# Optimization experiments

Hardware: AMD Instinct MI355X
Metric: run time of the kernel (lower is better)

Reference implementation:

```python
import jax, jax.numpy as jnp
import numpy as np

B, C, L, K, R = 32, 64, 16384, 3, 8

def _lrelu(x):
    return jnp.where(x >= 0, x, 0.1 * x)

def setup_inputs() -> dict:
    key = jax.random.key(0)
    ks = jax.random.split(key, 8)
    s = lambda i, shape: (jax.random.normal(ks[i], shape, jnp.float32) * 0.05)
    return {
        "x0": jax.random.normal(ks[0], (B, C, L), jnp.float32),
        "x1": jax.random.normal(ks[1], (B, 64), jnp.float32),
        "W1": s(2, (64, 64)),           # Linear(64,64).weight [out,in]
        "W2": s(3, (64 * K, 64)),       # Linear(64,64*K).weight
        "conv_w": s(4, (C, C)),         # 1x1 Conv1d weight [out,in]
        "conv_b": s(5, (C,)),
        "ca_w1": s(6, (C // R, C)),     # CA conv1 weight
        "ca_w2": s(7, (C, C // R)),     # CA conv2 weight
    }

def reference(x0, x1, W1, W2, conv_w, conv_b, ca_w1, ca_w2):
    b, c, l = x0.shape
    k = W2.shape[0] // 64
    pad = (k - 1) // 2
    # dynamic per-(b,c) depthwise kernels
    h = _lrelu(x1 @ W1.T)                         # [b,64]
    kern = (h @ W2.T).reshape(b, c, k)            # [b,c,k]
    # depthwise conv1d (cross-correlation), groups=b*c
    xp = jnp.pad(x0, ((0, 0), (0, 0), (pad, pad)))
    out = sum(xp[:, :, j:j + l] * kern[:, :, j:j + 1] for j in range(k))
    out = _lrelu(out)
    # 1x1 conv
    out = jnp.einsum('bcl,oc->bol', out, conv_w) + conv_b[None, :, None]
    # channel attention gate on x1
    att = jax.nn.sigmoid(_lrelu(x1 @ ca_w1.T) @ ca_w2.T)  # [b,c]
    return out + x0 * att[:, :, None]
```

## Files before the change

kernel.cpp:

```cpp
#include <hip/hip_runtime.h>
#include <math.h>

#define B_ 32
#define C_ 64
#define L_ 16384
#define LT 64
#define NT 8
#define NBUF 3
#define NBLK (B_ * (L_ / (LT * NT)))

typedef __attribute__((ext_vector_type(8))) short short8;
typedef __attribute__((ext_vector_type(4))) float f32x4;

__device__ __forceinline__ unsigned short f2bf(float x) {
  unsigned int u = __builtin_bit_cast(unsigned int, x);
  u += 0x7fffu + ((u >> 16) & 1u);
  return (unsigned short)(u >> 16);
}

__device__ __forceinline__ float lrelu(float x) {
  return x >= 0.f ? x : 0.1f * x;
}

__device__ __forceinline__ void load_lds_16(const void* g, void* l) {
  __builtin_amdgcn_global_load_lds(
      (const __attribute__((address_space(1))) void*)g,
      (__attribute__((address_space(3))) void*)l, 16, 0, 0);
}

__global__ void da_prep(const float* __restrict__ x1,
                        const float* __restrict__ W1,
                        const float* __restrict__ W2,
                        const float* __restrict__ ca_w1,
                        const float* __restrict__ ca_w2,
                        const float* __restrict__ conv_w,
                        float* __restrict__ kern4,
                        float* __restrict__ att,
                        unsigned short* __restrict__ wfrag) {
  int b = blockIdx.x;
  int t = threadIdx.x;
  __shared__ float x1s[64], h[64], a1[8];
  x1s[t] = x1[b * 64 + t];
  __syncthreads();
  {
    const float* w1r = W1 + t * 64;
    float s = 0.f;
    #pragma unroll
    for (int i = 0; i < 64; ++i) s = fmaf(x1s[i], w1r[i], s);
    h[t] = lrelu(s);
  }
  if (t < 8) {
    const float* cw = ca_w1 + t * 64;
    float a = 0.f;
    #pragma unroll
    for (int i = 0; i < 64; ++i) a = fmaf(x1s[i], cw[i], a);
    a1[t] = lrelu(a);
  }
  __syncthreads();
  #pragma unroll
  for (int kk = 0; kk < 3; ++kk) {
    const float* w2r = W2 + (t * 3 + kk) * 64;
    float s2 = 0.f;
    #pragma unroll
    for (int i = 0; i < 64; ++i) s2 = fmaf(h[i], w2r[i], s2);
    kern4[(b * 64 + t) * 4 + kk] = s2;
  }
  kern4[(b * 64 + t) * 4 + 3] = 0.f;
  {
    float a = 0.f;
    #pragma unroll
    for (int r = 0; r < 8; ++r) a = fmaf(a1[r], ca_w2[t * 8 + r], a);
    att[b * 64 + t] = 1.f / (1.f + expf(-a));
  }
  if (b == 0) {
    #pragma unroll
    for (int kt = 0; kt < 2; ++kt)
      #pragma unroll
      for (int mt = 0; mt < 4; ++mt)
        #pragma unroll
        for (int j = 0; j < 8; ++j) {
          float e = conv_w[(mt * 16 + (t & 15)) * 64 + kt * 32 + (t >> 4) * 8 + j];
          wfrag[(((kt * 4 + mt) * 64) + t) * 8 + j] = f2bf(e);
        }
  }
}

__global__ __launch_bounds__(256, 2) void da_main(
    const float* __restrict__ x0,
    const float* __restrict__ conv_b,
    const float* __restrict__ kern4,
    const float* __restrict__ att,
    const unsigned short* __restrict__ wfrag,
    float* __restrict__ out) {
  __shared__ float x0s[NBUF][64 * LT];
  __shared__ unsigned short midT[LT * 64];
  __shared__ float haloL[2][64];

  int bid = blockIdx.x;
  int b = bid >> 5;
  int base_l = (bid & 31) * (NT * LT);
  int tid = threadIdx.x;
  int lane = tid & 63;
  int wave = tid >> 6;

  int m_lane = lane & 15;
  int kbase = (lane >> 4) * 8;
  int qq = lane >> 4;

  const float* xb = x0 + (size_t)(b * 64) * L_;

  auto STAGE = [&](int t1, int d) {
    int p = lane & 15;
    int r4r = lane >> 4;
    #pragma unroll
    for (int i = 0; i < 4; ++i) {
      int c = wave * 16 + i * 4 + r4r;
      const float* g = xb + (size_t)c * L_ + base_l + t1 * LT + ((p ^ (c & 7)) << 2);
      load_lds_16(g, &x0s[d][(wave * 16 + i * 4) * LT]);
    }
  };

  short8 af[2][4];
  #pragma unroll
  for (int kt = 0; kt < 2; ++kt)
    #pragma unroll
    for (int mt = 0; mt < 4; ++mt)
      af[kt][mt] = *(const short8*)&wfrag[(((kt * 4 + mt) * 64) + lane) * 8];

  float4 kv = *(const float4*)&kern4[(b * 64 + lane) * 4];
  float k0 = kv.x, k1 = kv.y, k2 = kv.z;

  float cb_r[4][4], at_r[4][4];
  #pragma unroll
  for (int mt = 0; mt < 4; ++mt)
    #pragma unroll
    for (int r = 0; r < 4; ++r) {
      int o = mt * 16 + qq * 4 + r;
      cb_r[mt][r] = conv_b[o];
      at_r[mt][r] = att[b * 64 + o];
    }

  float hl0 = 0.f, hnL = 0.f;
  if (wave == 0 && base_l > 0) hl0 = xb[(size_t)lane * L_ + base_l - 1];
  if (wave == 3 && base_l + NT * LT < L_)
    hnL = xb[(size_t)lane * L_ + base_l + NT * LT];

  if (wave == 0) haloL[0][lane] = hl0;
  __syncthreads();

  STAGE(0, 0);
  STAGE(1, 1);

  #pragma unroll
  for (int t = 0; t < NT; ++t) {
    const int d = t % NBUF;

    if (t + 2 < NT) STAGE(t + 2, (t + 2) % NBUF);

    if (t == 0)
      asm volatile("s_waitcnt vmcnt(4)" ::: "memory");
    else if (t + 2 < NT)
      asm volatile("s_waitcnt vmcnt(20)" ::: "memory");
    else if (t + 2 == NT)
      asm volatile("s_waitcnt vmcnt(16)" ::: "memory");
    __builtin_amdgcn_s_barrier();

    {
      int c = lane;
      int w0 = wave * 16;
      const float* row = &x0s[d][c * LT];
      const int csw = (c & 7) << 2;

      float4 q[4];
      #pragma unroll
      for (int i = 0; i < 4; ++i)
        q[i] = *(const float4*)&row[((wave * 4 + i) ^ (c & 7)) << 2];

      float prev, nxt;
      if (wave == 0) {
        prev = (t == 0) ? hl0 : haloL[t & 1][c];
      } else {
        int w = w0 - 1;
        prev = row[((w & ~3) ^ csw) + (w & 3)];
      }
      if (wave == 3) {
        nxt = (t == NT - 1) ? hnL
                            : x0s[(t + 1) % NBUF][c * LT + ((c & 7) << 2)];
      } else {
        int w = w0 + 16;
        nxt = row[((w & ~3) ^ csw) + (w & 3)];
      }

      if (t + 1 < NT && wave == 3) haloL[(t + 1) & 1][c] = q[3].w;

      #pragma unroll
      for (int i = 0; i < 4; ++i) {
        float xa = q[i].x, xb2 = q[i].y, xc = q[i].z, xd = q[i].w;
        float xm1 = prev;
        if (i > 0) xm1 = q[i - 1].w;
        float xp1 = nxt;
        if (i < 3) xp1 = q[i + 1].x;
        float m0 = fmaf(k0, xm1, fmaf(k1, xa,  k2 * xb2));
        float m1 = fmaf(k0, xa,  fmaf(k1, xb2, k2 * xc));
        float m2 = fmaf(k0, xb2, fmaf(k1, xc,  k2 * xd));
        float m3 = fmaf(k0, xc,  fmaf(k1, xd,  k2 * xp1));
        int l = w0 + 4 * i;
        midT[(l + 0) * 64 + (c ^ (((l + 0) & 7) << 3))] = f2bf(lrelu(m0));
        midT[(l + 1) * 64 + (c ^ (((l + 1) & 7) << 3))] = f2bf(lrelu(m1));
        midT[(l + 2) * 64 + (c ^ (((l + 2) & 7) << 3))] = f2bf(lrelu(m2));
        midT[(l + 3) * 64 + (c ^ (((l + 3) & 7) << 3))] = f2bf(lrelu(m3));
      }
    }

    f32x4 acc[4];
    #pragma unroll
    for (int mt = 0; mt < 4; ++mt) acc[mt] = (f32x4){0.f, 0.f, 0.f, 0.f};
    int l = wave * 16 + m_lane;
    #pragma unroll
    for (int kt = 0; kt < 2; ++kt) {
      int cb = kt * 32 + kbase;
      const short8 bf = *(const short8*)&midT[l * 64 + (cb ^ ((l & 7) << 3))];
      #pragma unroll
      for (int mt = 0; mt < 4; ++mt)
        acc[mt] = __builtin_amdgcn_mfma_f32_16x16x32_bf16(af[kt][mt], bf,
                                                          acc[mt], 0, 0, 0);
    }

    {
      int w = wave * 16 + m_lane;
      int l0t = base_l + t * LT;
      #pragma unroll
      for (int mt = 0; mt < 4; ++mt) {
        #pragma unroll
        for (int r = 0; r < 4; ++r) {
          int o = mt * 16 + qq * 4 + r;
          float xv = x0s[d][o * LT + (((w & ~3) ^ ((o & 7) << 2)) + (w & 3))];
          out[(size_t)(b * 64 + o) * L_ + l0t + w] =
              acc[mt][r] + cb_r[mt][r] + xv * at_r[mt][r];
        }
      }
    }

    if (t + 1 < NT) {
      asm volatile("s_waitcnt lgkmcnt(0)" ::: "memory");
      __builtin_amdgcn_s_barrier();
    }
  }
}

extern "C" void kernel_launch(void* const* d_in, const int* in_sizes, int n_in,
                              void* d_out, int out_size, void* d_ws, size_t ws_size,
                              hipStream_t stream) {
  const float* x0     = (const float*)d_in[0];
  const float* x1     = (const float*)d_in[1];
  const float* W1     = (const float*)d_in[2];
  const float* W2     = (const float*)d_in[3];
  const float* conv_w = (const float*)d_in[4];
  const float* conv_b = (const float*)d_in[5];
  const float* ca_w1  = (const float*)d_in[6];
  const float* ca_w2  = (const float*)d_in[7];
  float* out = (float*)d_out;

  float* kern4 = (float*)d_ws;
  float* att   = kern4 + B_ * C_ * 4;
  unsigned short* wfrag = (unsigned short*)(att + B_ * C_);

  da_prep<<<dim3(B_), dim3(64), 0, stream>>>(x1, W1, W2, ca_w1, ca_w2, conv_w,
                                             kern4, att, wfrag);
  da_main<<<dim3(NBLK), dim3(256), 0, stream>>>(x0, conv_b, kern4, att, wfrag,
                                                out);
}
```

Baseline: 64.98 us.

## Halve tile length, raise occupancy, split MFMA output channels across waves

The L tile shrinks from 64 to 32 and tiles per block go from 8 to 16. Launch bounds are raised to four blocks per CU, and the 1x1-conv MFMA work is re-split so each wave owns half the output channels for 16 positions. The goal is more resident waves and smaller LDS and register footprints, to hide the global latency of this memory-bound kernel. The cost is an extra barrier per tile, since waves now read midT rows written by other waves, plus a rolled loop with rotating buffer indices.

Result: no change. 63.80 us (-1.8%).

```diff
diff --git a/kernel.cpp b/kernel.cpp
--- a/kernel.cpp
+++ b/kernel.cpp
@@ -4,8 +4,8 @@
 #define B_ 32
 #define C_ 64
 #define L_ 16384
-#define LT 64
-#define NT 8
+#define LT 32
+#define NT 16
 #define NBUF 3
 #define NBLK (B_ * (L_ / (LT * NT)))
 
@@ -85,7 +85,7 @@
   }
 }
 
-__global__ __launch_bounds__(256, 2) void da_main(
+__global__ __launch_bounds__(256, 4) void da_main(
     const float* __restrict__ x0,
     const float* __restrict__ conv_b,
     const float* __restrict__ kern4,
@@ -104,147 +104,150 @@
   int wave = tid >> 6;
 
   int m_lane = lane & 15;
-  int kbase = (lane >> 4) * 8;
   int qq = lane >> 4;
+  int kbase = qq * 8;
+  int oh = wave >> 1;
+  int lh = wave & 1;
+  int wl = lh * 16 + m_lane;
 
   const float* xb = x0 + (size_t)(b * 64) * L_;
 
-  auto STAGE = [&](int t1, int d) {
-    int p = lane & 15;
-    int r4r = lane >> 4;
-    #pragma unroll
-    for (int i = 0; i < 4; ++i) {
-      int c = wave * 16 + i * 4 + r4r;
-      const float* g = xb + (size_t)c * L_ + base_l + t1 * LT + ((p ^ (c & 7)) << 2);
-      load_lds_16(g, &x0s[d][(wave * 16 + i * 4) * LT]);
+  auto STAGE = [&](int t1, int dd) {
+    #pragma unroll
+    for (int i = 0; i < 2; ++i) {
+      int rg = (wave * 2 + i) * 8;
+      int c = rg + (lane >> 3);
+      int g = (lane & 7) ^ (c & 7);
+      const float* gp = xb + (size_t)c * L_ + base_l + t1 * LT + g * 4;
+      load_lds_16(gp, &x0s[dd][rg * LT]);
     }
   };
 
-  short8 af[2][4];
+  short8 af[2][2];
   #pragma unroll
   for (int kt = 0; kt < 2; ++kt)
     #pragma unroll
-    for (int mt = 0; mt < 4; ++mt)
-      af[kt][mt] = *(const short8*)&wfrag[(((kt * 4 + mt) * 64) + lane) * 8];
+    for (int mt2 = 0; mt2 < 2; ++mt2)
+      af[kt][mt2] =
+          *(const short8*)&wfrag[(((kt * 4 + oh * 2 + mt2) * 64) + lane) * 8];
 
   float4 kv = *(const float4*)&kern4[(b * 64 + lane) * 4];
   float k0 = kv.x, k1 = kv.y, k2 = kv.z;
 
-  float cb_r[4][4], at_r[4][4];
+  float cb_r[2][4], at_r[2][4];
   #pragma unroll
-  for (int mt = 0; mt < 4; ++mt)
+  for (int mt2 = 0; mt2 < 2; ++mt2)
     #pragma unroll
     for (int r = 0; r < 4; ++r) {
-      int o = mt * 16 + qq * 4 + r;
-      cb_r[mt][r] = conv_b[o];
-      at_r[mt][r] = att[b * 64 + o];
+      int o = oh * 32 + mt2 * 16 + qq * 4 + r;
+      cb_r[mt2][r] = conv_b[o];
+      at_r[mt2][r] = att[b * 64 + o];
     }
 
   float hl0 = 0.f, hnL = 0.f;
   if (wave == 0 && base_l > 0) hl0 = xb[(size_t)lane * L_ + base_l - 1];
   if (wave == 3 && base_l + NT * LT < L_)
     hnL = xb[(size_t)lane * L_ + base_l + NT * LT];
-
   if (wave == 0) haloL[0][lane] = hl0;
+
   __syncthreads();
 
   STAGE(0, 0);
   STAGE(1, 1);
 
-  #pragma unroll
+  int cur = 0, nxt = 1, nx2 = 2;
   for (int t = 0; t < NT; ++t) {
-    const int d = t % NBUF;
-
-    if (t + 2 < NT) STAGE(t + 2, (t + 2) % NBUF);
+    if (t + 2 < NT) STAGE(t + 2, nx2);
 
     if (t == 0)
-      asm volatile("s_waitcnt vmcnt(4)" ::: "memory");
-    else if (t + 2 < NT)
-      asm volatile("s_waitcnt vmcnt(20)" ::: "memory");
-    else if (t + 2 == NT)
-      asm volatile("s_waitcnt vmcnt(16)" ::: "memory");
+      asm volatile("s_waitcnt vmcnt(2)" ::: "memory");
+    else if (t < NT - 2)
+      asm volatile("s_waitcnt vmcnt(10)" ::: "memory");
+    else if (t == NT - 2)
+      asm volatile("s_waitcnt vmcnt(8)" ::: "memory");
     __builtin_amdgcn_s_barrier();
 
     {
       int c = lane;
-      int w0 = wave * 16;
-      const float* row = &x0s[d][c * LT];
-      const int csw = (c & 7) << 2;
-
-      float4 q[4];
-      #pragma unroll
-      for (int i = 0; i < 4; ++i)
-        q[i] = *(const float4*)&row[((wave * 4 + i) ^ (c & 7)) << 2];
-
-      float prev, nxt;
+      int cs = c & 7;
+      const float* row = &x0s[cur][c * LT];
+
+      float4 q0 = *(const float4*)&row[((wave * 2 + 0) ^ cs) << 2];
+      float4 q1 = *(const float4*)&row[((wave * 2 + 1) ^ cs) << 2];
+
+      float prev, nxtv;
       if (wave == 0) {
         prev = (t == 0) ? hl0 : haloL[t & 1][c];
       } else {
-        int w = w0 - 1;
-        prev = row[((w & ~3) ^ csw) + (w & 3)];
+        prev = row[(((wave * 2 - 1) ^ cs) << 2) + 3];
       }
       if (wave == 3) {
-        nxt = (t == NT - 1) ? hnL
-                            : x0s[(t + 1) % NBUF][c * LT + ((c & 7) << 2)];
+        nxtv = (t == NT - 1) ? hnL : x0s[nxt][c * LT + (cs << 2)];
       } else {
-        int w = w0 + 16;
-        nxt = row[((w & ~3) ^ csw) + (w & 3)];
+        nxtv = row[((wave * 2 + 2) ^ cs) << 2];
       }
-
-      if (t + 1 < NT && wave == 3) haloL[(t + 1) & 1][c] = q[3].w;
-
+      if (wave == 3 && t + 1 < NT) haloL[(t + 1) & 1][c] = q1.w;
+
+      float m0 = fmaf(k0, prev, fmaf(k1, q0.x, k2 * q0.y));
+      float m1 = fmaf(k0, q0.x, fmaf(k1, q0.y, k2 * q0.z));
+      float m2 = fmaf(k0, q0.y, fmaf(k1, q0.z, k2 * q0.w));
+      float m3 = fmaf(k0, q0.z, fmaf(k1, q0.w, k2 * q1.x));
+      float m4 = fmaf(k0, q0.w, fmaf(k1, q1.x, k2 * q1.y));
+      float m5 = fmaf(k0, q1.x, fmaf(k1, q1.y, k2 * q1.z));
+      float m6 = fmaf(k0, q1.y, fmaf(k1, q1.z, k2 * q1.w));
+      float m7 = fmaf(k0, q1.z, fmaf(k1, q1.w, k2 * nxtv));
+
+      int lb = wave * 8;
+      midT[(lb + 0) * 64 + (c ^ (0 << 3))] = f2bf(lrelu(m0));
+      midT[(lb + 1) * 64 + (c ^ (1 << 3))] = f2bf(lrelu(m1));
+      midT[(lb + 2) * 64 + (c ^ (2 << 3))] = f2bf(lrelu(m2));
+      midT[(lb + 3) * 64 + (c ^ (3 << 3))] = f2bf(lrelu(m3));
+      midT[(lb + 4) * 64 + (c ^ (4 << 3))] = f2bf(lrelu(m4));
+      midT[(lb + 5) * 64 + (c ^ (5 << 3))] = f2bf(lrelu(m5));
+      midT[(lb + 6) * 64 + (c ^ (6 << 3))] = f2bf(lrelu(m6));
+      midT[(lb + 7) * 64 + (c ^ (7 << 3))] = f2bf(lrelu(m7));
+    }
+
+    float xv[2][4];
+    #pragma unroll
+    for (int mt2 = 0; mt2 < 2; ++mt2)
       #pragma unroll
-      for (int i = 0; i < 4; ++i) {
-        float xa = q[i].x, xb2 = q[i].y, xc = q[i].z, xd = q[i].w;
-        float xm1 = prev;
-        if (i > 0) xm1 = q[i - 1].w;
-        float xp1 = nxt;
-        if (i < 3) xp1 = q[i + 1].x;
-        float m0 = fmaf(k0, xm1, fmaf(k1, xa,  k2 * xb2));
-        float m1 = fmaf(k0, xa,  fmaf(k1, xb2, k2 * xc));
-        float m2 = fmaf(k0, xb2, fmaf(k1, xc,  k2 * xd));
-        float m3 = fmaf(k0, xc,  fmaf(k1, xd,  k2 * xp1));
-        int l = w0 + 4 * i;
-        midT[(l + 0) * 64 + (c ^ (((l + 0) & 7) << 3))] = f2bf(lrelu(m0));
-        midT[(l + 1) * 64 + (c ^ (((l + 1) & 7) << 3))] = f2bf(lrelu(m1));
-        midT[(l + 2) * 64 + (c ^ (((l + 2) & 7) << 3))] = f2bf(lrelu(m2));
-        midT[(l + 3) * 64 + (c ^ (((l + 3) & 7) << 3))] = f2bf(lrelu(m3));
+      for (int r = 0; r < 4; ++r) {
+        int o = oh * 32 + mt2 * 16 + qq * 4 + r;
+        xv[mt2][r] =
+            x0s[cur][o * LT + (((wl >> 2) ^ (o & 7)) << 2) + (wl & 3)];
       }
-    }
-
-    f32x4 acc[4];
-    #pragma unroll
-    for (int mt = 0; mt < 4; ++mt) acc[mt] = (f32x4){0.f, 0.f, 0.f, 0.f};
-    int l = wave * 16 + m_lane;
+
+    asm volatile("s_waitcnt lgkmcnt(0)" ::: "memory");
+    __builtin_amdgcn_s_barrier();
+
+    f32x4 acc[2];
+    acc[0] = (f32x4){0.f, 0.f, 0.f, 0.f};
+    acc[1] = (f32x4){0.f, 0.f, 0.f, 0.f};
     #pragma unroll
     for (int kt = 0; kt < 2; ++kt) {
       int cb = kt * 32 + kbase;
-      const short8 bf = *(const short8*)&midT[l * 64 + (cb ^ ((l & 7) << 3))];
+      const short8 bf =
+          *(const short8*)&midT[wl * 64 + (cb ^ ((wl & 7) << 3))];
+      acc[0] = __builtin_amdgcn_mfma_f32_16x16x32_bf16(af[kt][0], bf, acc[0],
+                                                       0, 0, 0);
+      acc[1] = __builtin_amdgcn_mfma_f32_16x16x32_bf16(af[kt][1], bf, acc[1],
+                                                       0, 0, 0);
+    }
+
+    {
+      size_t obase = (size_t)(b * 64) * L_ + base_l + t * LT + wl;
       #pragma unroll
-      for (int mt = 0; mt < 4; ++mt)
-        acc[mt] = __builtin_amdgcn_mfma_f32_16x16x32_bf16(af[kt][mt], bf,
-                                                          acc[mt], 0, 0, 0);
-    }
-
-    {
-      int w = wave * 16 + m_lane;
-      int l0t = base_l + t * LT;
-      #pragma unroll
-      for (int mt = 0; mt < 4; ++mt) {
+      for (int mt2 = 0; mt2 < 2; ++mt2)
         #pragma unroll
         for (int r = 0; r < 4; ++r) {
-          int o = mt * 16 + qq * 4 + r;
-          float xv = x0s[d][o * LT + (((w & ~3) ^ ((o & 7) << 2)) + (w & 3))];
-          out[(size_t)(b * 64 + o) * L_ + l0t + w] =
-              acc[mt][r] + cb_r[mt][r] + xv * at_r[mt][r];
+          int o = oh * 32 + mt2 * 16 + qq * 4 + r;
+          out[obase + (size_t)o * L_] =
+              acc[mt2][r] + cb_r[mt2][r] + xv[mt2][r] * at_r[mt2][r];
         }
-      }
-    }
-
-    if (t + 1 < NT) {
-      asm volatile("s_waitcnt lgkmcnt(0)" ::: "memory");
-      __builtin_amdgcn_s_barrier();
-    }
+    }
+
+    int tmp = cur; cur = nxt; nxt = nx2; nx2 = tmp;
   }
 }
 
```

## Reuse the x0 staging buffer for bf16 mid tiles and use one barrier per tile

Applied to the files above, without the earlier changes.

Drops the separate midT LDS array. The bf16 depthwise-conv output is now written into the x0 staging slot of the current tile, after the residual x values have been pulled into registers. This shrinks LDS per block so launch bounds can request 3 blocks per CU instead of 2. The tile loop is restructured around a single barrier, with the next prefetch issued after it and the buffer indices rotated rather than fully unrolled. The trade-offs are more live registers under a tighter register budget and a uniform, more conservative vmcnt wait that also counts pending stores.

After: 112.0 us. 72.3% more time.

```diff
diff --git a/kernel.cpp b/kernel.cpp
--- a/kernel.cpp
+++ b/kernel.cpp
@@ -85,7 +85,7 @@
   }
 }
 
-__global__ __launch_bounds__(256, 2) void da_main(
+__global__ __launch_bounds__(256, 3) void da_main(
     const float* __restrict__ x0,
     const float* __restrict__ conv_b,
     const float* __restrict__ kern4,
@@ -93,7 +93,6 @@
     const unsigned short* __restrict__ wfrag,
     float* __restrict__ out) {
   __shared__ float x0s[NBUF][64 * LT];
-  __shared__ unsigned short midT[LT * 64];
   __shared__ float haloL[2][64];
 
   int bid = blockIdx.x;
@@ -104,21 +103,26 @@
   int wave = tid >> 6;
 
   int m_lane = lane & 15;
-  int kbase = (lane >> 4) * 8;
   int qq = lane >> 4;
+  int kbase = qq * 8;
+  int wl = wave * 16 + m_lane;
+  int cs = lane & 7;
 
   const float* xb = x0 + (size_t)(b * 64) * L_;
 
-  auto STAGE = [&](int t1, int d) {
-    int p = lane & 15;
-    int r4r = lane >> 4;
+  auto STAGE = [&](int t1, int dd) {
     #pragma unroll
     for (int i = 0; i < 4; ++i) {
-      int c = wave * 16 + i * 4 + r4r;
-      const float* g = xb + (size_t)c * L_ + base_l + t1 * LT + ((p ^ (c & 7)) << 2);
-      load_lds_16(g, &x0s[d][(wave * 16 + i * 4) * LT]);
+      int rg = wave * 16 + i * 4;
+      int c = rg + (lane >> 4);
+      int p = (lane & 15) ^ (c & 7);
+      const float* gp = xb + (size_t)c * L_ + base_l + t1 * LT + (p << 2);
+      load_lds_16(gp, &x0s[dd][rg * LT]);
     }
   };
+
+  STAGE(0, 0);
+  STAGE(1, 1);
 
   short8 af[2][4];
   #pragma unroll
@@ -144,107 +148,91 @@
   if (wave == 0 && base_l > 0) hl0 = xb[(size_t)lane * L_ + base_l - 1];
   if (wave == 3 && base_l + NT * LT < L_)
     hnL = xb[(size_t)lane * L_ + base_l + NT * LT];
-
   if (wave == 0) haloL[0][lane] = hl0;
+
   __syncthreads();
 
-  STAGE(0, 0);
-  STAGE(1, 1);
-
-  #pragma unroll
+  int cur = 0, nx1 = 1, nx2 = 2;
   for (int t = 0; t < NT; ++t) {
-    const int d = t % NBUF;
-
-    if (t + 2 < NT) STAGE(t + 2, (t + 2) % NBUF);
-
-    if (t == 0)
-      asm volatile("s_waitcnt vmcnt(4)" ::: "memory");
-    else if (t + 2 < NT)
-      asm volatile("s_waitcnt vmcnt(20)" ::: "memory");
-    else if (t + 2 == NT)
-      asm volatile("s_waitcnt vmcnt(16)" ::: "memory");
+    asm volatile("s_waitcnt vmcnt(16)" ::: "memory");
+
+    const float* row = &x0s[cur][lane * LT];
+    float4 q[4];
+    #pragma unroll
+    for (int i = 0; i < 4; ++i)
+      q[i] = *(const float4*)&row[((4 * wave + i) ^ cs) << 2];
+
+    float prev;
+    if (wave == 0) prev = haloL[t & 1][lane];
+    else           prev = row[(((4 * wave - 1) ^ cs) << 2) + 3];
+    float nxtv = 0.f;
+    if (wave != 3) nxtv = row[((4 * wave + 4) ^ cs) << 2];
+    if (wave == 3) haloL[(t + 1) & 1][lane] = q[3].w;
+
+    float xv[4][4];
+    #pragma unroll
+    for (int mt = 0; mt < 4; ++mt)
+      #pragma unroll
+      for (int r = 0; r < 4; ++r) {
+        int o = mt * 16 + qq * 4 + r;
+        xv[mt][r] =
+            x0s[cur][o * LT + (((wl >> 2) ^ (o & 7)) << 2) + (wl & 3)];
+      }
+
+    asm volatile("s_waitcnt lgkmcnt(0)" ::: "memory");
     __builtin_amdgcn_s_barrier();
+    asm volatile("" ::: "memory");
+
+    if (t + 2 < NT) STAGE(t + 2, nx2);
+
+    if (wave == 3)
+      nxtv = (t == NT - 1) ? hnL : x0s[nx1][lane * LT + (cs << 2)];
 
     {
-      int c = lane;
-      int w0 = wave * 16;
-      const float* row = &x0s[d][c * LT];
-      const int csw = (c & 7) << 2;
-
-      float4 q[4];
-      #pragma unroll
-      for (int i = 0; i < 4; ++i)
-        q[i] = *(const float4*)&row[((wave * 4 + i) ^ (c & 7)) << 2];
-
-      float prev, nxt;
-      if (wave == 0) {
-        prev = (t == 0) ? hl0 : haloL[t & 1][c];
-      } else {
-        int w = w0 - 1;
-        prev = row[((w & ~3) ^ csw) + (w & 3)];
+      unsigned short* mid = (unsigned short*)&x0s[cur][0];
+      float xa[16] = {q[0].x, q[0].y, q[0].z, q[0].w, q[1].x, q[1].y,
+                      q[1].z, q[1].w, q[2].x, q[2].y, q[2].z, q[2].w,
+                      q[3].x, q[3].y, q[3].z, q[3].w};
+      int lb = wave * 16;
+      #pragma unroll
+      for (int j = 0; j < 16; ++j) {
+        float xm = (j == 0) ? prev : xa[j - 1];
+        float xp = (j == 15) ? nxtv : xa[j + 1];
+        float m = fmaf(k0, xm, fmaf(k1, xa[j], k2 * xp));
+        mid[(lb + j) * 64 + (lane ^ ((j & 7) << 3))] = f2bf(lrelu(m));
       }
-      if (wave == 3) {
-        nxt = (t == NT - 1) ? hnL
-                            : x0s[(t + 1) % NBUF][c * LT + ((c & 7) << 2)];
-      } else {
-        int w = w0 + 16;
-        nxt = row[((w & ~3) ^ csw) + (w & 3)];
+    }
+
+    f32x4 acc[4];
+    #pragma unroll
+    for (int mt = 0; mt < 4; ++mt) acc[mt] = (f32x4){0.f, 0.f, 0.f, 0.f};
+    {
+      const unsigned short* mid = (const unsigned short*)&x0s[cur][0];
+      #pragma unroll
+      for (int kt = 0; kt < 2; ++kt) {
+        int cb = kt * 32 + kbase;
+        const short8 bf =
+            *(const short8*)&mid[wl * 64 + (cb ^ ((wl & 7) << 3))];
+        #pragma unroll
+        for (int mt = 0; mt < 4; ++mt)
+          acc[mt] = __builtin_amdgcn_mfma_f32_16x16x32_bf16(af[kt][mt], bf,
+                                                            acc[mt], 0, 0, 0);
       }
-
-      if (t + 1 < NT && wave == 3) haloL[(t + 1) & 1][c] = q[3].w;
-
-      #pragma unroll
-      for (int i = 0; i < 4; ++i) {
-        float xa = q[i].x, xb2 = q[i].y, xc = q[i].z, xd = q[i].w;
-        float xm1 = prev;
-        if (i > 0) xm1 = q[i - 1].w;
-        float xp1 = nxt;
-        if (i < 3) xp1 = q[i + 1].x;
-        float m0 = fmaf(k0, xm1, fmaf(k1, xa,  k2 * xb2));
-        float m1 = fmaf(k0, xa,  fmaf(k1, xb2, k2 * xc));
-        float m2 = fmaf(k0, xb2, fmaf(k1, xc,  k2 * xd));
-        float m3 = fmaf(k0, xc,  fmaf(k1, xd,  k2 * xp1));
-        int l = w0 + 4 * i;
-        midT[(l + 0) * 64 + (c ^ (((l + 0) & 7) << 3))] = f2bf(lrelu(m0));
-        midT[(l + 1) * 64 + (c ^ (((l + 1) & 7) << 3))] = f2bf(lrelu(m1));
-        midT[(l + 2) * 64 + (c ^ (((l + 2) & 7) << 3))] = f2bf(lrelu(m2));
-        midT[(l + 3) * 64 + (c ^ (((l + 3) & 7) << 3))] = f2bf(lrelu(m3));
-      }
-    }
-
-    f32x4 acc[4];
-    #pragma unroll
-    for (int mt = 0; mt < 4; ++mt) acc[mt] = (f32x4){0.f, 0.f, 0.f, 0.f};
-    int l = wave * 16 + m_lane;
-    #pragma unroll
-    for (int kt = 0; kt < 2; ++kt) {
-      int cb = kt * 32 + kbase;
-      const short8 bf = *(const short8*)&midT[l * 64 + (cb ^ ((l & 7) << 3))];
+    }
+
+    {
+      size_t obase = (size_t)(b * 64) * L_ + base_l + t * LT + wl;
       #pragma unroll
       for (int mt = 0; mt < 4; ++mt)
-        acc[mt] = __builtin_amdgcn_mfma_f32_16x16x32_bf16(af[kt][mt], bf,
-                                                          acc[mt], 0, 0, 0);
-    }
-
-    {
-      int w = wave * 16 + m_lane;
-      int l0t = base_l + t * LT;
-      #pragma unroll
-      for (int mt = 0; mt < 4; ++mt) {
         #pragma unroll
         for (int r = 0; r < 4; ++r) {
           int o = mt * 16 + qq * 4 + r;
-          float xv = x0s[d][o * LT + (((w & ~3) ^ ((o & 7) << 2)) + (w & 3))];
-          out[(size_t)(b * 64 + o) * L_ + l0t + w] =
-              acc[mt][r] + cb_r[mt][r] + xv * at_r[mt][r];
+          out[obase + (size_t)o * L_] =
+              acc[mt][r] + cb_r[mt][r] + xv[mt][r] * at_r[mt][r];
         }
-      }
-    }
-
-    if (t + 1 < NT) {
-      asm volatile("s_waitcnt lgkmcnt(0)" ::: "memory");
-      __builtin_amdgcn_s_barrier();
-    }
+    }
+
+    int tmp = cur; cur = nx1; nx1 = nx2; nx2 = tmp;
   }
 }
 
```
